# Kernel tuning notes

Measured on AMD Instinct MI355X. Metric: run time of the kernel, lower is better.

Reference implementation:

```python
import jax, jax.numpy as jnp
import numpy as np

WAY, SHOT, HEADS = 5, 5, 12
DIM, L = 768, 512
HD = DIM // HEADS  # 64
SCALE = 1.0 / (HD ** 0.5)


def _layernorm(x, g, b, eps=1e-5):
    m = jnp.mean(x, axis=-1, keepdims=True)
    v = jnp.var(x, axis=-1, keepdims=True)
    return (x - m) / jnp.sqrt(v + eps) * g + b


def setup_inputs() -> dict:
    key = jax.random.key(0)
    ks = jax.random.split(key, 7)
    x = jax.random.normal(ks[0], (WAY * SHOT, L, DIM), dtype=jnp.float32)
    Wq = 0.02 * jax.random.normal(ks[1], (DIM, DIM), dtype=jnp.float32)
    Wk = 0.02 * jax.random.normal(ks[2], (DIM, DIM), dtype=jnp.float32)
    Wv = 0.02 * jax.random.normal(ks[3], (DIM, DIM), dtype=jnp.float32)
    Wo = 0.02 * jax.random.normal(ks[4], (DIM, DIM), dtype=jnp.float32)
    wp = 0.02 * jax.random.normal(ks[5], (DIM,), dtype=jnp.float32)
    return {
        "x": x,
        "Wq": Wq, "bq": jnp.zeros((DIM,), jnp.float32),
        "Wk": Wk, "bk": jnp.zeros((DIM,), jnp.float32),
        "Wv": Wv, "bv": jnp.zeros((DIM,), jnp.float32),
        "gamma": jnp.ones((DIM,), jnp.float32),
        "beta": jnp.zeros((DIM,), jnp.float32),
        "wp": wp, "bp": jnp.zeros((), jnp.float32),
        "Wo": Wo, "bo": jnp.zeros((DIM,), jnp.float32),
    }


def reference(x, Wq, bq, Wk, bk, Wv, bv, gamma, beta, wp, bp, Wo, bo):
    # flag == 'XS' branch; mask=None; dropout in eval mode (identity).
    x = x.reshape(WAY, SHOT, L, DIM)
    # projections -> (way, heads, shot, l, head_dim)
    q = (x @ Wq.T + bq).reshape(WAY, SHOT, L, HEADS, HD).transpose(0, 3, 1, 2, 4)
    k = (x @ Wk.T + bk).reshape(WAY, SHOT, L, HEADS, HD).transpose(0, 3, 1, 2, 4)
    v = (x @ Wv.T + bv).reshape(WAY, SHOT, L, HEADS, HD).transpose(0, 3, 1, 2, 4)

    # branch 1: standard token attention, scores (w,h,s,l,l)
    s1 = jnp.einsum('whsld,whsmd->whslm', q, k) * SCALE
    w1 = jax.nn.softmax(s1, axis=-1)
    o1 = jnp.einsum('whslm,whsmd->whsld', w1, v)
    o1 = o1.transpose(0, 2, 3, 1, 4).reshape(WAY, SHOT, L, DIM)  # (w,s,l,h*d)
    a1 = jnp.max(o1, axis=2)  # max-pool over tokens -> (w,s,dim)

    # branch 2: transposed 'channel' attention across shots, scores (w,h,d,s,s)
    s2 = jnp.einsum('whsld,whtld->whdst', q, k) * SCALE
    w2 = jax.nn.softmax(s2, axis=-1)
    o2 = jnp.einsum('whdst,whtld->whdsl', w2, v)
    o2 = o2.transpose(0, 3, 4, 1, 2).reshape(WAY, SHOT, L, DIM)  # (w,s,l,h*d)
    a2 = jnp.max(o2, axis=2)  # (w,s,dim)

    attn = (_layernorm(a1, gamma, beta) + _layernorm(a2, gamma, beta)) * 0.5
    proto = jnp.tanh(attn)
    pw = jax.nn.softmax(proto @ wp + bp, axis=-1)[..., None]  # softmax over shots
    proto = pw * attn
    proto = proto @ Wo.T + bo
    return jnp.sum(proto, axis=1)  # (way, dim)
```

## Files before the change

### kernel.cpp

```cpp
#include <hip/hip_runtime.h>
#include <math.h>

#define WAY 5
#define SHOT 5
#define HEADS 12
#define DIM 768
#define LSEQ 512
#define HD 64
#define NROWS (WAY*SHOT*LSEQ)
#define SCALE 0.125f
#define NXEL ((size_t)NROWS*DIM)
#define NWEL ((size_t)DIM*DIM)

typedef __attribute__((ext_vector_type(8))) short short8;
typedef __attribute__((ext_vector_type(4))) float f32x4;
typedef __attribute__((ext_vector_type(4))) unsigned short ushort4v;

__device__ __forceinline__ float bf2f(unsigned short u) {
    union { unsigned int i; float f; } x; x.i = ((unsigned int)u) << 16; return x.f;
}
__device__ __forceinline__ unsigned short f2bf(float f) {
    union { float f; unsigned int i; } x; x.f = f;
    unsigned int r = x.i + 0x7FFFu + ((x.i >> 16) & 1u);
    return (unsigned short)(r >> 16);
}

#define NX4 (NROWS*DIM/4)
#define NW4 (DIM*DIM/4)
__global__ __launch_bounds__(256) void cast_all(
    const float* __restrict__ X, const float* __restrict__ Wq,
    const float* __restrict__ Wk, const float* __restrict__ Wv,
    unsigned short* __restrict__ Xb, unsigned short* __restrict__ Wb)
{
    int i = blockIdx.x * 256 + threadIdx.x;
    const float* s; unsigned short* d; int off;
    if (i < NX4)               { s = X;  d = Xb;            off = i; }
    else if (i < NX4 + NW4)    { s = Wq; d = Wb;            off = i - NX4; }
    else if (i < NX4 + 2*NW4)  { s = Wk; d = Wb + NWEL;     off = i - NX4 - NW4; }
    else if (i < NX4 + 3*NW4)  { s = Wv; d = Wb + 2*NWEL;   off = i - NX4 - 2*NW4; }
    else return;
    float4 f = ((const float4*)s)[off];
    ushort4v o;
    o.x = f2bf(f.x); o.y = f2bf(f.y); o.z = f2bf(f.z); o.w = f2bf(f.w);
    *(ushort4v*)(d + (size_t)off*4) = o;
}

__global__ __launch_bounds__(256) void qkv_mfma(
    const unsigned short* __restrict__ Xb, const unsigned short* __restrict__ Wball,
    const float* __restrict__ bq, const float* __restrict__ bk, const float* __restrict__ bv,
    unsigned short* __restrict__ qkv_out)
{
    const int bid  = blockIdx.x;
    const int sw   = (bid & 7) * 225 + (bid >> 3);
    const int mblk = sw / 18;
    const int nblk = sw - mblk * 18;
    const int m0   = mblk * 128;
    const int n0g  = nblk * 128;
    const int which = n0g / DIM;
    const int n0    = n0g - which * DIM;

    const unsigned short* W = Wball + (size_t)n0g * DIM;
    const float* bias = (which == 0) ? bq : ((which == 1) ? bk : bv);
    unsigned short* out = qkv_out + (size_t)which * NXEL;

    __shared__ __align__(16) unsigned short Sm[4][128*64];

    const int t = threadIdx.x;
    const int w = t >> 6;
    const int lane = t & 63;
    const int quad = lane >> 4;
    const int l15 = lane & 15;
    const int wm = (w & 1) * 64;
    const int wn = (w >> 1) * 64;

    const int srow   = lane >> 3;
    const int gchunk = (lane & 7) ^ srow;

    const unsigned short* gAbase = Xb + (size_t)(m0 + w*32 + srow)*DIM + gchunk*8;
    const unsigned short* gBbase = W  + (size_t)(w*32 + srow)*DIM      + gchunk*8;

    f32x4 acc[4][4];
    #pragma unroll
    for (int i = 0; i < 4; i++)
        #pragma unroll
        for (int j = 0; j < 4; j++)
            acc[i][j] = (f32x4){0.f, 0.f, 0.f, 0.f};

    #define STAGE(KT, BUF)                                                        \
        {                                                                         \
            _Pragma("unroll")                                                     \
            for (int c = 0; c < 4; c++) {                                         \
                __builtin_amdgcn_global_load_lds(                                 \
                    (const __attribute__((address_space(1))) unsigned int*)       \
                        (gAbase + (size_t)(c*8)*DIM + (KT)*64),                   \
                    (__attribute__((address_space(3))) unsigned int*)             \
                        &Sm[(BUF)*2][(w*32 + c*8)*64], 16, 0, 0);                 \
                __builtin_amdgcn_global_load_lds(                                 \
                    (const __attribute__((address_space(1))) unsigned int*)       \
                        (gBbase + (size_t)(c*8)*DIM + (KT)*64),                   \
                    (__attribute__((address_space(3))) unsigned int*)             \
                        &Sm[(BUF)*2 + 1][(w*32 + c*8)*64], 16, 0, 0);             \
            }                                                                     \
        }

    STAGE(0, 0);
    __syncthreads();

    #pragma unroll
    for (int kt = 0; kt < 12; ++kt) {
        if (kt + 1 < 12) STAGE(kt + 1, (kt + 1) & 1);

        const unsigned short* As = &Sm[(kt & 1) * 2][0];
        const unsigned short* Bs = &Sm[(kt & 1) * 2 + 1][0];

        #pragma unroll
        for (int kk = 0; kk < 2; kk++) {
            const int ch = kk*4 + quad;
            short8 af[4], bf_[4];
            #pragma unroll
            for (int i = 0; i < 4; i++) {
                const int row = wm + i*16 + l15;
                af[i]  = *(const short8*)&As[row*64 + ((ch ^ (row & 7)) << 3)];
            }
            #pragma unroll
            for (int j = 0; j < 4; j++) {
                const int row = wn + j*16 + l15;
                bf_[j] = *(const short8*)&Bs[row*64 + ((ch ^ (row & 7)) << 3)];
            }
            #pragma unroll
            for (int i = 0; i < 4; i++)
                #pragma unroll
                for (int j = 0; j < 4; j++)
                    acc[i][j] = __builtin_amdgcn_mfma_f32_16x16x32_bf16(af[i], bf_[j], acc[i][j], 0, 0, 0);
        }
        __syncthreads();
    }
    #undef STAGE

    unsigned short* Cs = &Sm[0][0];
    #pragma unroll
    for (int j = 0; j < 4; j++) {
        const int col = wn + j*16 + l15;
        const float bv_ = bias[n0 + col];
        #pragma unroll
        for (int i = 0; i < 4; i++) {
            #pragma unroll
            for (int r = 0; r < 4; r++) {
                const int row = wm + i*16 + quad*4 + r;
                Cs[row*136 + col] = f2bf(acc[i][j][r] + bv_);
            }
        }
    }
    __syncthreads();
    #pragma unroll
    for (int u = 0; u < 8; u++) {
        const int idx = u*256 + t;
        const int row = idx >> 4, ch = idx & 15;
        short8 v = *(const short8*)&Cs[row*136 + ch*8];
        *(short8*)&out[(size_t)(m0 + row)*DIM + n0 + ch*8] = v;
    }
}

__device__ __forceinline__ int swz(int row, int u) {
    return row*64 + ((u ^ (row & 7)) << 3);
}

__global__ __launch_bounds__(256) void attn1_mfma(
    const unsigned short* __restrict__ qb, const unsigned short* __restrict__ kb,
    const unsigned short* __restrict__ vb, float* __restrict__ a1p)
{
    int whs = blockIdx.x;
    const int chunk = blockIdx.y;
    const int si = whs % SHOT;  whs /= SHOT;
    const int hi = whs % HEADS; whs /= HEADS;
    const int wi = whs;
    const size_t baseRow = (size_t)(wi*SHOT + si) * LSEQ;
    const int colBase = hi * HD;

    __shared__ __align__(16) unsigned short Qs[64*64];
    __shared__ __align__(16) unsigned short Ks[64*64];
    __shared__ __align__(16) unsigned short Vt[64*64];
    __shared__ __align__(16) unsigned short Pb[64*64];
    __shared__ float cmaxs[4][64];

    const int t = threadIdx.x;
    const int w = t >> 6;
    const int lane = t & 63;
    const int quad = lane >> 4;
    const int l15 = lane & 15;

    #pragma unroll
    for (int p = 0; p < 2; p++) {
        int idx = p*256 + t;
        int row = idx >> 3, u = idx & 7;
        *(short8*)&Qs[swz(row, u)] =
            *(const short8*)&qb[(baseRow + chunk*64 + row)*DIM + colBase + u*8];
    }

    float l_part[4] = {0.f, 0.f, 0.f, 0.f};
    f32x4 o_acc[4];
    #pragma unroll
    for (int d = 0; d < 4; d++) o_acc[d] = (f32x4){0.f, 0.f, 0.f, 0.f};

    for (int kt = 0; kt < 8; kt++) {
        __syncthreads();
        #pragma unroll
        for (int p = 0; p < 2; p++) {
            int idx = p*256 + t;
            int row = idx >> 3, u = idx & 7;
            *(short8*)&Ks[swz(row, u)] =
                *(const short8*)&kb[(baseRow + kt*64 + row)*DIM + colBase + u*8];
        }
        #pragma unroll
        for (int p = 0; p < 2; p++) {
            int idx = p*256 + t;
            int d = idx & 63, lc = idx >> 6;
            unsigned short tmp[8];
            #pragma unroll
            for (int jj = 0; jj < 8; jj++)
                tmp[jj] = vb[(baseRow + kt*64 + lc*8 + jj)*DIM + colBase + d];
            *(short8*)&Vt[swz(d, lc)] = *(const short8*)tmp;
        }
        __syncthreads();

        f32x4 s_acc[4];
        #pragma unroll
        for (int nt = 0; nt < 4; nt++) s_acc[nt] = (f32x4){0.f, 0.f, 0.f, 0.f};
        short8 aq[2];
        #pragma unroll
        for (int kk = 0; kk < 2; kk++)
            aq[kk] = *(const short8*)&Qs[swz(w*16 + l15, kk*4 + quad)];
        #pragma unroll
        for (int kk = 0; kk < 2; kk++) {
            #pragma unroll
            for (int nt = 0; nt < 4; nt++) {
                short8 bk_ = *(const short8*)&Ks[swz(nt*16 + l15, kk*4 + quad)];
                s_acc[nt] = __builtin_amdgcn_mfma_f32_16x16x32_bf16(aq[kk], bk_, s_acc[nt], 0, 0, 0);
            }
        }

        #pragma unroll
        for (int nt = 0; nt < 4; nt++) {
            #pragma unroll
            for (int r = 0; r < 4; r++) {
                float e = __expf(s_acc[nt][r] * SCALE);
                s_acc[nt][r] = e;
                l_part[r] += e;
            }
        }

        #pragma unroll
        for (int nt = 0; nt < 4; nt++) {
            int ucol = nt*2 + (l15 >> 3);
            int cofs = l15 & 7;
            #pragma unroll
            for (int r = 0; r < 4; r++) {
                int row = w*16 + quad*4 + r;
                Pb[swz(row, ucol) + cofs] = f2bf(s_acc[nt][r]);
            }
        }

        short8 ap[2];
        #pragma unroll
        for (int kk = 0; kk < 2; kk++)
            ap[kk] = *(const short8*)&Pb[swz(w*16 + l15, kk*4 + quad)];
        #pragma unroll
        for (int kk = 0; kk < 2; kk++) {
            #pragma unroll
            for (int dt = 0; dt < 4; dt++) {
                short8 bv_ = *(const short8*)&Vt[swz(dt*16 + l15, kk*4 + quad)];
                o_acc[dt] = __builtin_amdgcn_mfma_f32_16x16x32_bf16(ap[kk], bv_, o_acc[dt], 0, 0, 0);
            }
        }
    }

    float l_tot[4];
    #pragma unroll
    for (int r = 0; r < 4; r++) {
        float s = l_part[r];
        #pragma unroll
        for (int off = 1; off < 16; off <<= 1) s += __shfl_xor(s, off);
        l_tot[r] = s;
    }

    float cm[4];
    #pragma unroll
    for (int dt = 0; dt < 4; dt++) {
        float mx = -1e30f;
        #pragma unroll
        for (int r = 0; r < 4; r++) mx = fmaxf(mx, o_acc[dt][r] / l_tot[r]);
        mx = fmaxf(mx, __shfl_xor(mx, 16));
        mx = fmaxf(mx, __shfl_xor(mx, 32));
        cm[dt] = mx;
    }
    if (quad == 0) {
        #pragma unroll
        for (int dt = 0; dt < 4; dt++) cmaxs[w][dt*16 + l15] = cm[dt];
    }
    __syncthreads();
    if (t < 64) {
        float mx = fmaxf(fmaxf(cmaxs[0][t], cmaxs[1][t]), fmaxf(cmaxs[2][t], cmaxs[3][t]));
        a1p[((size_t)((wi*HEADS + hi)*SHOT + si)*8 + chunk)*64 + t] = mx;
    }
}

__global__ __launch_bounds__(256) void attn2_scores(
    const unsigned short* __restrict__ qb, const unsigned short* __restrict__ kb,
    float* __restrict__ P1)
{
    const int wh = blockIdx.x, ch = blockIdx.y;
    const int wi = wh / HEADS, hi = wh % HEADS;
    const int t = threadIdx.x;
    const int doct = t & 7;
    const int pr = t >> 3;
    if (pr >= 25) return;
    const int si = pr / 5, tt = pr % 5;
    const int colB = hi*HD + doct*8;

    const unsigned short* qrow = qb + ((size_t)(wi*SHOT+si)*LSEQ + ch*64)*DIM + colB;
    const unsigned short* krow = kb + ((size_t)(wi*SHOT+tt)*LSEQ + ch*64)*DIM + colB;

    float acc[8] = {};
    #pragma unroll 8
    for (int l = 0; l < 64; l++) {
        short8 q8 = *(const short8*)(qrow + (size_t)l*DIM);
        short8 k8 = *(const short8*)(krow + (size_t)l*DIM);
        #pragma unroll
        for (int j = 0; j < 8; j++)
            acc[j] += bf2f((unsigned short)q8[j]) * bf2f((unsigned short)k8[j]);
    }
    #pragma unroll
    for (int j = 0; j < 8; j++)
        P1[((size_t)(wh*25 + pr)*64 + doct*8 + j)*8 + ch] = acc[j];
}

__global__ __launch_bounds__(320) void attn2_pmax(
    const float* __restrict__ P1, const unsigned short* __restrict__ vb,
    float* __restrict__ P2)
{
    const int wh = blockIdx.x, ch = blockIdx.y;
    const int wi = wh / HEADS, hi = wh % HEADS;
    const int t = threadIdx.x;
    const int si = t / 64;
    const int r  = t & 63;
    const int doct = r >> 3, lsub = r & 7;

    __shared__ float ssc[SHOT*SHOT*HD];

    for (int e = t; e < SHOT*SHOT*HD; e += 320) {
        const float* p = P1 + (size_t)(wh*25)*64*8 + (size_t)e*8;
        float s = 0.f;
        #pragma unroll
        for (int c = 0; c < 8; c++) s += p[c];
        ssc[e] = s * SCALE;
    }
    __syncthreads();

    float wgt[SHOT][8];
    #pragma unroll
    for (int j = 0; j < 8; j++) {
        const int d = doct*8 + j;
        float sum = 0.f;
        #pragma unroll
        for (int tt = 0; tt < SHOT; tt++) {
            float e = __expf(ssc[(si*SHOT + tt)*HD + d]);
            wgt[tt][j] = e; sum += e;
        }
        const float inv = 1.f / sum;
        #pragma unroll
        for (int tt = 0; tt < SHOT; tt++) wgt[tt][j] *= inv;
    }

    const int colB = hi*HD + doct*8;
    float m[8];
    #pragma unroll
    for (int j = 0; j < 8; j++) m[j] = -1e30f;

    #pragma unroll 4
    for (int lc = 0; lc < 8; lc++) {
        const int l = ch*64 + lsub*8 + lc;
        float val[8] = {};
        #pragma unroll
        for (int tt = 0; tt < SHOT; tt++) {
            short8 v8 = *(const short8*)(vb + ((size_t)(wi*SHOT+tt)*LSEQ + l)*DIM + colB);
            #pragma unroll
            for (int j = 0; j < 8; j++)
                val[j] += wgt[tt][j] * bf2f((unsigned short)v8[j]);
        }
        #pragma unroll
        for (int j = 0; j < 8; j++) m[j] = fmaxf(m[j], val[j]);
    }

    #pragma unroll
    for (int off = 1; off < 8; off <<= 1)
        #pragma unroll
        for (int j = 0; j < 8; j++) m[j] = fmaxf(m[j], __shfl_xor(m[j], off));

    if (lsub == 0) {
        #pragma unroll
        for (int j = 0; j < 8; j++)
            P2[((size_t)(wh*SHOT + si)*64 + doct*8 + j)*8 + ch] = m[j];
    }
}

__global__ __launch_bounds__(256) void combine(
    const float* __restrict__ a1p, const float* __restrict__ P2,
    const float* __restrict__ gamma, const float* __restrict__ beta,
    const float* __restrict__ wp, const float* __restrict__ bp,
    float* __restrict__ attn_ws, float* __restrict__ logits)
{
    const int wi = blockIdx.x / SHOT;
    const int si = blockIdx.x % SHOT;
    const int t  = threadIdx.x;

    __shared__ float row1[DIM];
    __shared__ float row2[DIM];
    __shared__ float rbuf[4][4];

    for (int j = t; j < DIM; j += 256) {
        int h = j / HD, d = j % HD;
        const float* p1 = a1p + ((size_t)((wi*HEADS + h)*SHOT + si) * 8) * 64 + d;
        float mx = -1e30f;
        #pragma unroll
        for (int c = 0; c < 8; c++) mx = fmaxf(mx, p1[c * 64]);
        row1[j] = mx;
        const float4* p2v = (const float4*)(P2 + ((size_t)((wi*HEADS + h)*SHOT + si)*64 + d)*8);
        const float4 pa = p2v[0], pb = p2v[1];
        float mx2 = fmaxf(fmaxf(fmaxf(pa.x, pa.y), fmaxf(pa.z, pa.w)),
                          fmaxf(fmaxf(pb.x, pb.y), fmaxf(pb.z, pb.w)));
        row2[j] = mx2;
    }
    __syncthreads();

    float s1 = 0, q1 = 0, s2 = 0, q2 = 0;
    for (int j = t; j < DIM; j += 256) {
        float x1 = row1[j]; s1 += x1; q1 += x1*x1;
        float x2 = row2[j]; s2 += x2; q2 += x2*x2;
    }
    #pragma unroll
    for (int off = 32; off > 0; off >>= 1) {
        s1 += __shfl_down(s1, off); q1 += __shfl_down(q1, off);
        s2 += __shfl_down(s2, off); q2 += __shfl_down(q2, off);
    }
    const int wid = t / 64, lane = t % 64;
    if (lane == 0) { rbuf[wid][0] = s1; rbuf[wid][1] = q1; rbuf[wid][2] = s2; rbuf[wid][3] = q2; }
    __syncthreads();
    if (t == 0) {
        float a = 0, b = 0, c = 0, dd = 0;
        #pragma unroll
        for (int i = 0; i < 4; i++) { a += rbuf[i][0]; b += rbuf[i][1]; c += rbuf[i][2]; dd += rbuf[i][3]; }
        rbuf[0][0] = a; rbuf[0][1] = b; rbuf[0][2] = c; rbuf[0][3] = dd;
    }
    __syncthreads();
    const float mean1 = rbuf[0][0] / (float)DIM;
    const float var1  = rbuf[0][1] / (float)DIM - mean1*mean1;
    const float mean2 = rbuf[0][2] / (float)DIM;
    const float var2  = rbuf[0][3] / (float)DIM - mean2*mean2;
    const float inv1 = rsqrtf(var1 + 1e-5f);
    const float inv2 = rsqrtf(var2 + 1e-5f);

    float dotp = 0.0f;
    for (int j = t; j < DIM; j += 256) {
        float v1 = (row1[j] - mean1) * inv1 * gamma[j] + beta[j];
        float v2 = (row2[j] - mean2) * inv2 * gamma[j] + beta[j];
        float at = 0.5f * (v1 + v2);
        attn_ws[(size_t)(wi*SHOT + si) * DIM + j] = at;
        dotp += tanhf(at) * wp[j];
    }
    #pragma unroll
    for (int off = 32; off > 0; off >>= 1) dotp += __shfl_down(dotp, off);
    __syncthreads();
    if (lane == 0) rbuf[wid][0] = dotp;
    __syncthreads();
    if (t == 0)
        logits[wi*SHOT + si] = rbuf[0][0] + rbuf[1][0] + rbuf[2][0] + rbuf[3][0] + bp[0];
}

__global__ __launch_bounds__(256) void outproj(
    const float* __restrict__ attn_ws, const float* __restrict__ logits,
    const float* __restrict__ Wo, const float* __restrict__ bo,
    float* __restrict__ out)
{
    const int t = threadIdx.x;
    __shared__ __align__(16) float P[WAY][DIM];

    float swt[WAY][SHOT];
    #pragma unroll
    for (int w5 = 0; w5 < WAY; w5++) {
        float lg[SHOT];
        float mx = -1e30f;
        #pragma unroll
        for (int s = 0; s < SHOT; s++) { lg[s] = logits[w5*SHOT + s]; mx = fmaxf(mx, lg[s]); }
        float sum = 0.f;
        #pragma unroll
        for (int s = 0; s < SHOT; s++) { lg[s] = __expf(lg[s] - mx); sum += lg[s]; }
        const float inv = 1.f / sum;
        #pragma unroll
        for (int s = 0; s < SHOT; s++) swt[w5][s] = lg[s] * inv;
    }

    #pragma unroll
    for (int c = 0; c < 3; c++) {
        const int d = c*256 + t;
        #pragma unroll
        for (int w5 = 0; w5 < WAY; w5++) {
            float a = 0.f;
            #pragma unroll
            for (int s = 0; s < SHOT; s++)
                a += swt[w5][s] * attn_ws[(size_t)(w5*SHOT + s)*DIM + d];
            P[w5][d] = a;
        }
    }
    __syncthreads();

    const int wid = t >> 6, lane = t & 63;
    const int j = blockIdx.x * 4 + wid;

    float acc[WAY] = {0.f, 0.f, 0.f, 0.f, 0.f};
    #pragma unroll
    for (int c = 0; c < 3; c++) {
        const int d = c*256 + lane*4;
        const float4 wo = *(const float4*)&Wo[(size_t)j*DIM + d];
        #pragma unroll
        for (int w5 = 0; w5 < WAY; w5++) {
            const float4 p = *(const float4*)&P[w5][d];
            acc[w5] += p.x*wo.x + p.y*wo.y + p.z*wo.z + p.w*wo.w;
        }
    }
    #pragma unroll
    for (int off = 32; off > 0; off >>= 1)
        #pragma unroll
        for (int w5 = 0; w5 < WAY; w5++)
            acc[w5] += __shfl_down(acc[w5], off);

    if (lane == 0) {
        const float b5 = 5.0f * bo[j];
        #pragma unroll
        for (int w5 = 0; w5 < WAY; w5++)
            out[(size_t)w5*DIM + j] = acc[w5] + b5;
    }
}

extern "C" void kernel_launch(void* const* d_in, const int* in_sizes, int n_in,
                              void* d_out, int out_size, void* d_ws, size_t ws_size,
                              hipStream_t stream) {
    const float* X     = (const float*)d_in[0];
    const float* Wq    = (const float*)d_in[1];
    const float* bq    = (const float*)d_in[2];
    const float* Wk    = (const float*)d_in[3];
    const float* bk    = (const float*)d_in[4];
    const float* Wv    = (const float*)d_in[5];
    const float* bv    = (const float*)d_in[6];
    const float* gamma = (const float*)d_in[7];
    const float* beta  = (const float*)d_in[8];
    const float* wp    = (const float*)d_in[9];
    const float* bp    = (const float*)d_in[10];
    const float* Wo    = (const float*)d_in[11];
    const float* bo    = (const float*)d_in[12];
    float* out = (float*)d_out;

    unsigned short* Xb   = (unsigned short*)d_ws;
    unsigned short* Wb   = Xb + NXEL;
    unsigned short* qkvb = Wb + 3*NWEL;
    unsigned short* qb = qkvb;
    unsigned short* kb = qkvb + NXEL;
    unsigned short* vb = qkvb + 2*NXEL;

    float* a1p    = (float*)(qkvb + 3*NXEL);
    float* P1     = a1p + (size_t)WAY*HEADS*SHOT*8*64;
    float* P2     = P1 + (size_t)WAY*HEADS*SHOT*SHOT*64*8;
    float* attn_b = P2 + (size_t)WAY*HEADS*SHOT*64*8;
    float* logits = attn_b + (size_t)WAY*SHOT*DIM;

    const int castN = NX4 + 3*NW4;
    cast_all<<<(castN + 255)/256, 256, 0, stream>>>(X, Wq, Wk, Wv, Xb, Wb);

    qkv_mfma<<<1800, 256, 0, stream>>>(Xb, Wb, bq, bk, bv, qkvb);

    dim3 g2(WAY*HEADS*SHOT, 8);
    attn1_mfma<<<g2, 256, 0, stream>>>(qb, kb, vb, a1p);

    dim3 g3(WAY*HEADS, 8);
    attn2_scores<<<g3, 256, 0, stream>>>(qb, kb, P1);
    attn2_pmax<<<g3, 320, 0, stream>>>(P1, vb, P2);

    combine<<<WAY*SHOT, 256, 0, stream>>>(a1p, P2, gamma, beta, wp, bp, attn_b, logits);
    outproj<<<192, 256, 0, stream>>>(attn_b, logits, Wo, bo, out);
}
```

Measured before the change: 274.4 us.

## Repartition channel-attention score kernel to one block per shot pair with in-block reduction

The attn2_scores kernel previously ran 480 blocks with only 200 of 256 threads active, each summing 64 tokens and writing 8 partial sums per element for attn2_pmax to reduce. It now launches 1500 blocks, one per (way, head, shot pair). All four waves stride over the 512 tokens, reduce through shuffles and shared memory, and write the final scaled score directly. This raises parallelism and drops the partial-sum buffer traffic. The cost is that q/k rows are now re-read per shot pair across more blocks, and a block-level sync is added.

```diff
diff --git a/kernel.cpp b/kernel.cpp
--- a/kernel.cpp
+++ b/kernel.cpp
@@ -306,23 +306,25 @@
 
 __global__ __launch_bounds__(256) void attn2_scores(
     const unsigned short* __restrict__ qb, const unsigned short* __restrict__ kb,
-    float* __restrict__ P1)
+    float* __restrict__ SSC)
 {
-    const int wh = blockIdx.x, ch = blockIdx.y;
+    const int bid = blockIdx.x;
+    const int wh = bid / 25, pr = bid % 25;
     const int wi = wh / HEADS, hi = wh % HEADS;
+    const int si = pr / 5, tt = pr % 5;
     const int t = threadIdx.x;
-    const int doct = t & 7;
-    const int pr = t >> 3;
-    if (pr >= 25) return;
-    const int si = pr / 5, tt = pr % 5;
+    const int w = t >> 6, lane = t & 63;
+    const int doct = lane & 7;
+    const int lgrp = w*8 + (lane >> 3);
     const int colB = hi*HD + doct*8;
 
-    const unsigned short* qrow = qb + ((size_t)(wi*SHOT+si)*LSEQ + ch*64)*DIM + colB;
-    const unsigned short* krow = kb + ((size_t)(wi*SHOT+tt)*LSEQ + ch*64)*DIM + colB;
+    const unsigned short* qrow = qb + (size_t)(wi*SHOT+si)*LSEQ*DIM + colB;
+    const unsigned short* krow = kb + (size_t)(wi*SHOT+tt)*LSEQ*DIM + colB;
 
     float acc[8] = {};
-    #pragma unroll 8
-    for (int l = 0; l < 64; l++) {
+    #pragma unroll
+    for (int it = 0; it < 16; it++) {
+        const int l = lgrp + it*32;
         short8 q8 = *(const short8*)(qrow + (size_t)l*DIM);
         short8 k8 = *(const short8*)(krow + (size_t)l*DIM);
         #pragma unroll
@@ -330,12 +332,26 @@
             acc[j] += bf2f((unsigned short)q8[j]) * bf2f((unsigned short)k8[j]);
     }
     #pragma unroll
-    for (int j = 0; j < 8; j++)
-        P1[((size_t)(wh*25 + pr)*64 + doct*8 + j)*8 + ch] = acc[j];
+    for (int off = 8; off < 64; off <<= 1)
+        #pragma unroll
+        for (int j = 0; j < 8; j++)
+            acc[j] += __shfl_xor(acc[j], off);
+
+    __shared__ float ws[4][8][8];
+    if (lane < 8) {
+        #pragma unroll
+        for (int j = 0; j < 8; j++) ws[w][lane][j] = acc[j];
+    }
+    __syncthreads();
+    if (t < 64) {
+        const int dct = t >> 3, j = t & 7;
+        float s = ws[0][dct][j] + ws[1][dct][j] + ws[2][dct][j] + ws[3][dct][j];
+        SSC[(size_t)(wh*25 + pr)*64 + dct*8 + j] = s * SCALE;
+    }
 }
 
 __global__ __launch_bounds__(320) void attn2_pmax(
-    const float* __restrict__ P1, const unsigned short* __restrict__ vb,
+    const float* __restrict__ SSC, const unsigned short* __restrict__ vb,
     float* __restrict__ P2)
 {
     const int wh = blockIdx.x, ch = blockIdx.y;
@@ -347,13 +363,8 @@
 
     __shared__ float ssc[SHOT*SHOT*HD];
 
-    for (int e = t; e < SHOT*SHOT*HD; e += 320) {
-        const float* p = P1 + (size_t)(wh*25)*64*8 + (size_t)e*8;
-        float s = 0.f;
-        #pragma unroll
-        for (int c = 0; c < 8; c++) s += p[c];
-        ssc[e] = s * SCALE;
-    }
+    for (int e = t; e < SHOT*SHOT*HD; e += 320)
+        ssc[e] = SSC[(size_t)wh*(SHOT*SHOT*HD) + e];
     __syncthreads();
 
     float wgt[SHOT][8];
@@ -567,8 +578,8 @@
     unsigned short* vb = qkvb + 2*NXEL;
 
     float* a1p    = (float*)(qkvb + 3*NXEL);
-    float* P1     = a1p + (size_t)WAY*HEADS*SHOT*8*64;
-    float* P2     = P1 + (size_t)WAY*HEADS*SHOT*SHOT*64*8;
+    float* SSC    = a1p + (size_t)WAY*HEADS*SHOT*8*64;
+    float* P2     = SSC + (size_t)WAY*HEADS*SHOT*SHOT*64*8;
     float* attn_b = P2 + (size_t)WAY*HEADS*SHOT*64*8;
     float* logits = attn_b + (size_t)WAY*SHOT*DIM;
 
@@ -580,9 +591,9 @@
     dim3 g2(WAY*HEADS*SHOT, 8);
     attn1_mfma<<<g2, 256, 0, stream>>>(qb, kb, vb, a1p);
 
+    attn2_scores<<<1500, 256, 0, stream>>>(qb, kb, SSC);
     dim3 g3(WAY*HEADS, 8);
-    attn2_scores<<<g3, 256, 0, stream>>>(qb, kb, P1);
-    attn2_pmax<<<g3, 320, 0, stream>>>(P1, vb, P2);
+    attn2_pmax<<<g3, 320, 0, stream>>>(SSC, vb, P2);
 
     combine<<<WAY*SHOT, 256, 0, stream>>>(a1p, P2, gamma, beta, wp, bp, attn_b, logits);
     outproj<<<192, 256, 0, stream>>>(attn_b, logits, Wo, bo, out);
```

Result: faster. 263.4 us, median of 2 (-4.0%).
